# Optimization experiments

Measured on AMD Instinct MI355X. Metric: run time of the kernel, lower is better.

The kernel has to match this reference:

```python
import jax, jax.numpy as jnp
import numpy as np

BETA = 0.95
THR = 1.0  # snntorch Leaky default threshold

# Heaviside spike with ATan surrogate gradient (snntorch default, alpha=2):
# d/dx = 1 / (1 + (pi*x)^2)
@jax.custom_vjp
def spike_fn(x):
    return (x > 0).astype(x.dtype)

def _spike_fwd(x):
    return spike_fn(x), x

def _spike_bwd(x, g):
    return (g / (1.0 + (jnp.pi * x) ** 2),)

spike_fn.defvjp(_spike_fwd, _spike_bwd)


def setup_inputs() -> dict:
    key = jax.random.key(0)
    ks = jax.random.split(key, 5)
    T, B, D_in, D_h, D_out = 25, 4096, 784, 1000, 10
    x = jax.random.normal(ks[0], (T, B, D_in), dtype=jnp.float32)
    # Kaiming-uniform-ish init like nn.Linear
    w1 = jax.random.uniform(ks[1], (D_h, D_in), jnp.float32, -1, 1) / np.sqrt(D_in)
    b1 = jax.random.uniform(ks[2], (D_h,), jnp.float32, -1, 1) / np.sqrt(D_in)
    w2 = jax.random.uniform(ks[3], (D_out, D_h), jnp.float32, -1, 1) / np.sqrt(D_h)
    b2 = jax.random.uniform(ks[4], (D_out,), jnp.float32, -1, 1) / np.sqrt(D_h)
    return {"x": x, "w1": w1, "b1": b1, "w2": w2, "b2": b2}


def reference(x, w1, b1, w2, b2):
    B = x.shape[1]
    mem1_0 = jnp.zeros((B, w1.shape[0]), x.dtype)
    mem2_0 = jnp.zeros((B, w2.shape[0]), x.dtype)

    def step(carry, xt):
        mem1, mem2 = carry
        # layer 1: Linear + Leaky (reset-by-subtraction, reset from prior mem)
        cur1 = xt @ w1.T + b1
        reset1 = spike_fn(mem1 - THR)
        mem1 = BETA * mem1 + cur1 - reset1 * THR
        spk1 = spike_fn(mem1 - THR)
        # layer 2
        cur2 = spk1 @ w2.T + b2
        reset2 = spike_fn(mem2 - THR)
        mem2 = BETA * mem2 + cur2 - reset2 * THR
        spk2 = spike_fn(mem2 - THR)
        return (mem1, mem2), spk2

    (mem1, mem2), spk_rec = jax.lax.scan(step, (mem1_0, mem2_0), x)
    return spk_rec, mem2
```

## Files before the change

### kernel.cpp

```cpp
#include <hip/hip_runtime.h>

typedef _Float16 f16;
typedef _Float16 f16x4 __attribute__((ext_vector_type(4)));
typedef _Float16 f16x8 __attribute__((ext_vector_type(8)));
typedef float f32x4 __attribute__((ext_vector_type(4)));

#define T_STEPS 25
#define BATCH   4096
#define DIN     784
#define DH      1000
#define HP      1024
#define DOUT    10
#define MROWS   (T_STEPS * BATCH)
#define KSEG    800
#define KA      (2 * KSEG)
#define KB      (3 * KSEG)
#define WROW    2432
#define NT64    38

__global__ void aconv_kernel(const float* __restrict__ x, f16* __restrict__ Ah)
{
    const int total = MROWS * 200;
    for (int idx = blockIdx.x * blockDim.x + threadIdx.x; idx < total;
         idx += gridDim.x * blockDim.x) {
        const int r  = idx / 200;
        const int c4 = (idx - r * 200) * 4;
        f16x4 hi, lo;
        if (c4 < DIN) {
            const float4 v = *(const float4*)(x + (size_t)r * DIN + c4);
            const float vv[4] = {v.x, v.y, v.z, v.w};
            #pragma unroll
            for (int j = 0; j < 4; ++j) {
                f16 h = (f16)vv[j];
                hi[j] = h;
                lo[j] = (f16)(vv[j] - (float)h);
            }
        } else {
            #pragma unroll
            for (int j = 0; j < 4; ++j) { hi[j] = (f16)0.f; lo[j] = (f16)0.f; }
        }
        *(f16x4*)(Ah + (size_t)r * KA + c4)        = hi;
        *(f16x4*)(Ah + (size_t)r * KA + KSEG + c4) = lo;
    }
}

__global__ void wconv_kernel(const float* __restrict__ w1, const float* __restrict__ b1,
                             const float* __restrict__ w2,
                             f16* __restrict__ Wh, float* __restrict__ b1p,
                             float* __restrict__ w2t)
{
    const int stride = gridDim.x * blockDim.x;
    const int tid0 = blockIdx.x * blockDim.x + threadIdx.x;
    for (int idx = tid0; idx < HP * WROW; idx += stride) {
        const int n  = idx / WROW;
        const int k  = idx - n * WROW;
        f16 v = (f16)0.f;
        if (k < KB) {
            const int seg = k / KSEG;
            const int kc  = k - seg * KSEG;
            float w = (n < DH && kc < DIN) ? w1[n * DIN + kc] : 0.f;
            f16 h = (f16)w;
            v = (seg < 2) ? h : (f16)(w - (float)h);
        }
        Wh[idx] = v;
    }
    for (int idx = tid0; idx < HP; idx += stride)
        b1p[idx] = (idx < DH) ? b1[idx] : 0.f;
    for (int idx = tid0; idx < HP * DOUT; idx += stride) {
        const int h = idx / DOUT;
        const int o = idx - h * DOUT;
        w2t[idx] = (h < DH) ? w2[o * DH + h] : 0.f;
    }
}

#define GL(gp, ldsoff) __builtin_amdgcn_global_load_lds( \
    (const __attribute__((address_space(1))) void*)(gp), \
    (__attribute__((address_space(3))) void*)(lds + (ldsoff)), 16, 0, 0)

#define STAGE64(tt) do { \
    const int _buf = ((tt) & 1) * 16384; \
    const int _ak  = (((tt) < 25) ? (tt) : ((tt) - 25)) * 64; \
    const int _bk  = (tt) * 64; \
    GL(Ag + _ak + 0 * 64 * KA,   _buf + 0 * 4096 + widoff); \
    GL(Ag + _ak + 1 * 64 * KA,   _buf + 1 * 4096 + widoff); \
    GL(Ag + _ak + 2 * 64 * KA,   _buf + 2 * 4096 + widoff); \
    GL(Ag + _ak + 3 * 64 * KA,   _buf + 3 * 4096 + widoff); \
    GL(Bg + _bk + 0 * 64 * WROW, 32768 + _buf + 0 * 4096 + widoff); \
    GL(Bg + _bk + 1 * 64 * WROW, 32768 + _buf + 1 * 4096 + widoff); \
    GL(Bg + _bk + 2 * 64 * WROW, 32768 + _buf + 2 * 4096 + widoff); \
    GL(Bg + _bk + 3 * 64 * WROW, 32768 + _buf + 3 * 4096 + widoff); } while (0)

#define MFMA16(A0, A1, A2, A3, B0, B1, B2, B3, M0) \
    acc[M0+0][0] = __builtin_amdgcn_mfma_f32_16x16x32_f16(A0, B0, acc[M0+0][0], 0, 0, 0); \
    acc[M0+0][1] = __builtin_amdgcn_mfma_f32_16x16x32_f16(A0, B1, acc[M0+0][1], 0, 0, 0); \
    acc[M0+0][2] = __builtin_amdgcn_mfma_f32_16x16x32_f16(A0, B2, acc[M0+0][2], 0, 0, 0); \
    acc[M0+0][3] = __builtin_amdgcn_mfma_f32_16x16x32_f16(A0, B3, acc[M0+0][3], 0, 0, 0); \
    acc[M0+1][0] = __builtin_amdgcn_mfma_f32_16x16x32_f16(A1, B0, acc[M0+1][0], 0, 0, 0); \
    acc[M0+1][1] = __builtin_amdgcn_mfma_f32_16x16x32_f16(A1, B1, acc[M0+1][1], 0, 0, 0); \
    acc[M0+1][2] = __builtin_amdgcn_mfma_f32_16x16x32_f16(A1, B2, acc[M0+1][2], 0, 0, 0); \
    acc[M0+1][3] = __builtin_amdgcn_mfma_f32_16x16x32_f16(A1, B3, acc[M0+1][3], 0, 0, 0); \
    acc[M0+2][0] = __builtin_amdgcn_mfma_f32_16x16x32_f16(A2, B0, acc[M0+2][0], 0, 0, 0); \
    acc[M0+2][1] = __builtin_amdgcn_mfma_f32_16x16x32_f16(A2, B1, acc[M0+2][1], 0, 0, 0); \
    acc[M0+2][2] = __builtin_amdgcn_mfma_f32_16x16x32_f16(A2, B2, acc[M0+2][2], 0, 0, 0); \
    acc[M0+2][3] = __builtin_amdgcn_mfma_f32_16x16x32_f16(A2, B3, acc[M0+2][3], 0, 0, 0); \
    acc[M0+3][0] = __builtin_amdgcn_mfma_f32_16x16x32_f16(A3, B0, acc[M0+3][0], 0, 0, 0); \
    acc[M0+3][1] = __builtin_amdgcn_mfma_f32_16x16x32_f16(A3, B1, acc[M0+3][1], 0, 0, 0); \
    acc[M0+3][2] = __builtin_amdgcn_mfma_f32_16x16x32_f16(A3, B2, acc[M0+3][2], 0, 0, 0); \
    acc[M0+3][3] = __builtin_amdgcn_mfma_f32_16x16x32_f16(A3, B3, acc[M0+3][3], 0, 0, 0);

#define RD(off) (*(const f16x8*)(lds + (off)))

#define BODY64(tt, STG) do { \
    const int bufc = ((tt) & 1) * 16384; \
    f16x8 b00, b01, b02, b03, a00, a01, a02, a03, a10, a11, a12, a13; \
    f16x8 b10, b11, b12, b13, c00, c01, c02, c03, c10, c11, c12, c13; \
    if (STG) STAGE64((tt) + 1); \
     \
    b00 = RD(bbase + bufc + 0 * 1024 + cA0); \
    b01 = RD(bbase + bufc + 1 * 1024 + cA0); \
    b02 = RD(bbase + bufc + 2 * 1024 + cA0); \
    b03 = RD(bbase + bufc + 3 * 1024 + cA0); \
    a00 = RD(abase + bufc + 0 * 1024 + cA0); \
    a01 = RD(abase + bufc + 1 * 1024 + cA0); \
    a02 = RD(abase + bufc + 2 * 1024 + cA0); \
    a03 = RD(abase + bufc + 3 * 1024 + cA0); \
    a10 = RD(abase + bufc + 4096 + 0 * 1024 + cA0); \
    a11 = RD(abase + bufc + 4096 + 1 * 1024 + cA0); \
    a12 = RD(abase + bufc + 4096 + 2 * 1024 + cA0); \
    a13 = RD(abase + bufc + 4096 + 3 * 1024 + cA0); \
    asm volatile("s_waitcnt lgkmcnt(4)" ::: "memory");   \
    __builtin_amdgcn_sched_barrier(0); \
    __builtin_amdgcn_s_setprio(1); \
    MFMA16(a00, a01, a02, a03, b00, b01, b02, b03, 0) \
    __builtin_amdgcn_s_setprio(0); \
    asm volatile("s_waitcnt lgkmcnt(0)" ::: "memory");   \
    __builtin_amdgcn_sched_barrier(0); \
     \
    b10 = RD(bbase + bufc + 0 * 1024 + cA1); \
    b11 = RD(bbase + bufc + 1 * 1024 + cA1); \
    b12 = RD(bbase + bufc + 2 * 1024 + cA1); \
    b13 = RD(bbase + bufc + 3 * 1024 + cA1); \
    c00 = RD(abase + bufc + 0 * 1024 + cA1); \
    c01 = RD(abase + bufc + 1 * 1024 + cA1); \
    c02 = RD(abase + bufc + 2 * 1024 + cA1); \
    c03 = RD(abase + bufc + 3 * 1024 + cA1); \
    c10 = RD(abase + bufc + 4096 + 0 * 1024 + cA1); \
    c11 = RD(abase + bufc + 4096 + 1 * 1024 + cA1); \
    c12 = RD(abase + bufc + 4096 + 2 * 1024 + cA1); \
    c13 = RD(abase + bufc + 4096 + 3 * 1024 + cA1); \
    __builtin_amdgcn_sched_barrier(0); \
    __builtin_amdgcn_s_setprio(1); \
    MFMA16(a10, a11, a12, a13, b00, b01, b02, b03, 4) \
    __builtin_amdgcn_s_setprio(0); \
    asm volatile("s_waitcnt lgkmcnt(4)" ::: "memory");   \
    __builtin_amdgcn_sched_barrier(0); \
    __builtin_amdgcn_s_setprio(1); \
    MFMA16(c00, c01, c02, c03, b10, b11, b12, b13, 0) \
    __builtin_amdgcn_s_setprio(0); \
    asm volatile("s_waitcnt lgkmcnt(0)" ::: "memory");   \
    __builtin_amdgcn_sched_barrier(0); \
    __builtin_amdgcn_s_setprio(1); \
    MFMA16(c10, c11, c12, c13, b10, b11, b12, b13, 4) \
    __builtin_amdgcn_s_setprio(0); \
    if (STG) { \
        asm volatile("s_waitcnt vmcnt(0)" ::: "memory");   \
        __builtin_amdgcn_s_barrier(); \
    } \
} while (0)

__global__ __launch_bounds__(512, 2)
void gemm_kernel(const f16* __restrict__ A, const f16* __restrict__ B,
                 const float* __restrict__ bias, float* __restrict__ C)
{
    __shared__ f16 lds[65536];

    const int bid = blockIdx.x;
    const int swz = (bid & 7) * 200 + (bid >> 3);
    const int mt = swz >> 2;
    const int nt = swz & 3;
    const size_t rowBase = (size_t)mt * 256;
    const int colBase = nt * 256;

    const int tid  = threadIdx.x;
    const int wid  = tid >> 6;
    const int lane = tid & 63;
    const int wm = wid >> 2;
    const int wn = wid & 3;

    const int gsw = (tid & 7) ^ ((tid >> 3) & 7);
    const f16* Ag = A + (rowBase + (tid >> 3)) * KA + gsw * 8;
    const f16* Bg = B + (size_t)(colBase + (tid >> 3)) * WROW + gsw * 8;
    const int widoff = wid * 512;

    const int cA0 = (((lane >> 4))     ^ (lane & 7)) * 8;
    const int cA1 = (((lane >> 4) + 4) ^ (lane & 7)) * 8;
    const int abase = (wm * 128 + (lane & 15)) * 64;
    const int bbase = 32768 + (wn * 64 + (lane & 15)) * 64;

    f32x4 acc[8][4];
    #pragma unroll
    for (int m = 0; m < 8; ++m)
        #pragma unroll
        for (int n = 0; n < 4; ++n)
            acc[m][n] = (f32x4){0.f, 0.f, 0.f, 0.f};

    STAGE64(0);
    asm volatile("s_waitcnt vmcnt(0)" ::: "memory");
    __builtin_amdgcn_s_barrier();

    for (int t = 0; t < 36; t += 2) {
        BODY64(t, 1);
        BODY64(t + 1, 1);
    }
    BODY64(36, 1);
    BODY64(37, 0);

    const int c_col0 = colBase + wn * 64 + (lane & 15);
    const size_t c_row0 = rowBase + wm * 128 + (lane >> 4) * 4;
    #pragma unroll
    for (int n = 0; n < 4; ++n) {
        const int gcol = c_col0 + n * 16;
        const float bv = bias[gcol];
        #pragma unroll
        for (int m = 0; m < 8; ++m) {
            const size_t grow = c_row0 + m * 16;
            #pragma unroll
            for (int r = 0; r < 4; ++r)
                C[(grow + r) * HP + gcol] = acc[m][n][r] + bv;
        }
    }
}

__global__ __launch_bounds__(256)
void phase2_kernel(const float* __restrict__ cur1, const float* __restrict__ w2t,
                   const float* __restrict__ b2, float* __restrict__ out)
{
    __shared__ float w2s[HP * DOUT];
    const int tid = threadIdx.x;
    for (int i = tid; i < HP * DOUT; i += 256) w2s[i] = w2t[i];

    const int lane = tid & 63;
    const int wave = tid >> 6;
    const int b = blockIdx.x * 4 + wave;

    float m1[16];
    #pragma unroll
    for (int i = 0; i < 16; ++i) m1[i] = 0.f;
    float m2[DOUT], b2r[DOUT];
    #pragma unroll
    for (int o = 0; o < DOUT; ++o) { m2[o] = 0.f; b2r[o] = b2[o]; }
    __syncthreads();

    for (int t = 0; t < T_STEPS; ++t) {
        const float* cr = cur1 + ((size_t)t * BATCH + b) * HP;
        float p[DOUT];
        #pragma unroll
        for (int o = 0; o < DOUT; ++o) p[o] = 0.f;

        #pragma unroll
        for (int c = 0; c < 4; ++c) {
            const float4 cu = *(const float4*)(cr + c * 256 + lane * 4);
            const float cv[4] = {cu.x, cu.y, cu.z, cu.w};
            #pragma unroll
            for (int j = 0; j < 4; ++j) {
                const float mo = m1[c * 4 + j];
                const float rs = (mo > 1.0f) ? 1.0f : 0.0f;
                const float mn = 0.95f * mo + cv[j] - rs;
                m1[c * 4 + j] = mn;
                if (mn > 1.0f) {
                    const float* wr = w2s + (c * 256 + lane * 4 + j) * DOUT;
                    #pragma unroll
                    for (int o = 0; o < DOUT; ++o) p[o] += wr[o];
                }
            }
        }
        #pragma unroll
        for (int o = 0; o < DOUT; ++o) {
            float v = p[o];
            #pragma unroll
            for (int msk = 32; msk > 0; msk >>= 1) v += __shfl_xor(v, msk, 64);
            p[o] = v;
        }
        #pragma unroll
        for (int o = 0; o < DOUT; ++o) {
            const float cur2 = p[o] + b2r[o];
            const float mo = m2[o];
            const float rs = (mo > 1.0f) ? 1.0f : 0.0f;
            m2[o] = 0.95f * mo + cur2 - rs;
        }
        if (lane < DOUT)
            out[(size_t)t * (BATCH * DOUT) + (size_t)b * DOUT + lane] =
                (m2[lane] > 1.0f) ? 1.0f : 0.0f;
    }
    if (lane < DOUT)
        out[(size_t)T_STEPS * BATCH * DOUT + (size_t)b * DOUT + lane] = m2[lane];
}

extern "C" void kernel_launch(void* const* d_in, const int* in_sizes, int n_in,
                              void* d_out, int out_size, void* d_ws, size_t ws_size,
                              hipStream_t stream)
{
    const float* x  = (const float*)d_in[0];
    const float* w1 = (const float*)d_in[1];
    const float* b1 = (const float*)d_in[2];
    const float* w2 = (const float*)d_in[3];
    const float* b2 = (const float*)d_in[4];
    float* out = (float*)d_out;

    char* wsb = (char*)d_ws;
    f16*   Ah   = (f16*)(wsb);
    f16*   Wh   = (f16*)(wsb + 327680000);
    float* cur1 = (float*)(wsb + 327680000 + 4980736);
    float* b1p  = (float*)(wsb + 327680000 + 4980736 + 419430400);
    float* w2t  = (float*)(wsb + 327680000 + 4980736 + 419430400 + 4096);

    aconv_kernel<<<4096, 256, 0, stream>>>(x, Ah);
    wconv_kernel<<<1024, 256, 0, stream>>>(w1, b1, w2, Wh, b1p, w2t);
    gemm_kernel<<<1600, 512, 0, stream>>>(Ah, Wh, b1p, cur1);
    phase2_kernel<<<1024, 256, 0, stream>>>(cur1, w2t, b2, out);
}
```

Before: 746.7 us.

## Fuse fp32-to-split-fp16 conversion of x into the GEMM A-tile staging

```diff
diff --git a/kernel.cpp b/kernel.cpp
--- a/kernel.cpp
+++ b/kernel.cpp
@@ -1,7 +1,6 @@
 #include <hip/hip_runtime.h>
 
 typedef _Float16 f16;
-typedef _Float16 f16x4 __attribute__((ext_vector_type(4)));
 typedef _Float16 f16x8 __attribute__((ext_vector_type(8)));
 typedef float f32x4 __attribute__((ext_vector_type(4)));
 
@@ -13,36 +12,9 @@
 #define DOUT    10
 #define MROWS   (T_STEPS * BATCH)
 #define KSEG    800
-#define KA      (2 * KSEG)
 #define KB      (3 * KSEG)
 #define WROW    2432
 #define NT64    38
-
-__global__ void aconv_kernel(const float* __restrict__ x, f16* __restrict__ Ah)
-{
-    const int total = MROWS * 200;
-    for (int idx = blockIdx.x * blockDim.x + threadIdx.x; idx < total;
-         idx += gridDim.x * blockDim.x) {
-        const int r  = idx / 200;
-        const int c4 = (idx - r * 200) * 4;
-        f16x4 hi, lo;
-        if (c4 < DIN) {
-            const float4 v = *(const float4*)(x + (size_t)r * DIN + c4);
-            const float vv[4] = {v.x, v.y, v.z, v.w};
-            #pragma unroll
-            for (int j = 0; j < 4; ++j) {
-                f16 h = (f16)vv[j];
-                hi[j] = h;
-                lo[j] = (f16)(vv[j] - (float)h);
-            }
-        } else {
-            #pragma unroll
-            for (int j = 0; j < 4; ++j) { hi[j] = (f16)0.f; lo[j] = (f16)0.f; }
-        }
-        *(f16x4*)(Ah + (size_t)r * KA + c4)        = hi;
-        *(f16x4*)(Ah + (size_t)r * KA + KSEG + c4) = lo;
-    }
-}
 
 __global__ void wconv_kernel(const float* __restrict__ w1, const float* __restrict__ b1,
                              const float* __restrict__ w2,
@@ -77,19 +49,81 @@
     (const __attribute__((address_space(1))) void*)(gp), \
     (__attribute__((address_space(3))) void*)(lds + (ldsoff)), 16, 0, 0)
 
-#define STAGE64(tt) do { \
+#define AKOF(tt) ((((tt) < 25) ? (tt) : ((tt) - 25)) * 64)
+
+#define STAGE_B(tt) do { \
     const int _buf = ((tt) & 1) * 16384; \
-    const int _ak  = (((tt) < 25) ? (tt) : ((tt) - 25)) * 64; \
     const int _bk  = (tt) * 64; \
-    GL(Ag + _ak + 0 * 64 * KA,   _buf + 0 * 4096 + widoff); \
-    GL(Ag + _ak + 1 * 64 * KA,   _buf + 1 * 4096 + widoff); \
-    GL(Ag + _ak + 2 * 64 * KA,   _buf + 2 * 4096 + widoff); \
-    GL(Ag + _ak + 3 * 64 * KA,   _buf + 3 * 4096 + widoff); \
     GL(Bg + _bk + 0 * 64 * WROW, 32768 + _buf + 0 * 4096 + widoff); \
     GL(Bg + _bk + 1 * 64 * WROW, 32768 + _buf + 1 * 4096 + widoff); \
     GL(Bg + _bk + 2 * 64 * WROW, 32768 + _buf + 2 * 4096 + widoff); \
     GL(Bg + _bk + 3 * 64 * WROW, 32768 + _buf + 3 * 4096 + widoff); } while (0)
 
+#define ACOL(tt, c_, ldc_) \
+    const int c_    = AKOF(tt) + gsw8; \
+    const int _sc   = (c_ < 800) ? c_ : (c_ - 800); \
+    const int ldc_  = (_sc < 784) ? _sc : 0;
+
+#define LOADA01(tt) do { ACOL(tt, _c, _ldc) \
+    fa00 = *(const f32x4*)(Xrow + 0 * 64 * DIN + _ldc); \
+    fa01 = *(const f32x4*)(Xrow + 0 * 64 * DIN + _ldc + 4); \
+    fa10 = *(const f32x4*)(Xrow + 1 * 64 * DIN + _ldc); \
+    fa11 = *(const f32x4*)(Xrow + 1 * 64 * DIN + _ldc + 4); } while (0)
+#define LOADA23(tt) do { ACOL(tt, _c, _ldc) \
+    fa20 = *(const f32x4*)(Xrow + 2 * 64 * DIN + _ldc); \
+    fa21 = *(const f32x4*)(Xrow + 2 * 64 * DIN + _ldc + 4); \
+    fa30 = *(const f32x4*)(Xrow + 3 * 64 * DIN + _ldc); \
+    fa31 = *(const f32x4*)(Xrow + 3 * 64 * DIN + _ldc + 4); } while (0)
+
+#define CVT8(w_, va, vb) do { \
+    _Pragma("unroll") \
+    for (int _j = 0; _j < 4; ++_j) { \
+        float _v = va[_j]; \
+        f16 _h = (f16)_v; \
+        f16 _l = (f16)(_v - (float)_h); \
+        w_[_j] = _pad ? (f16)0.f : (_lo ? _l : _h); \
+    } \
+    _Pragma("unroll") \
+    for (int _j = 0; _j < 4; ++_j) { \
+        float _v = vb[_j]; \
+        f16 _h = (f16)_v; \
+        f16 _l = (f16)(_v - (float)_h); \
+        w_[4 + _j] = _pad ? (f16)0.f : (_lo ? _l : _h); \
+    } } while (0)
+
+#define CVTWR(tt) do { ACOL(tt, _c, _ldcu) (void)_ldcu; \
+    const int _sc2  = (_c < 800) ? _c : (_c - 800); \
+    const bool _lo  = (_c >= 800); \
+    const bool _pad = (_sc2 >= 784); \
+    const int _wb   = ((tt) & 1) * 16384 + tid * 8; \
+    f16x8 w0, w1_, w2_, w3_; \
+    CVT8(w0,  fa00, fa01); CVT8(w1_, fa10, fa11); \
+    CVT8(w2_, fa20, fa21); CVT8(w3_, fa30, fa31); \
+    *(f16x8*)(lds + _wb + 0 * 4096) = w0; \
+    *(f16x8*)(lds + _wb + 1 * 4096) = w1_; \
+    *(f16x8*)(lds + _wb + 2 * 4096) = w2_; \
+    *(f16x8*)(lds + _wb + 3 * 4096) = w3_; } while (0)
+
+#define MFMA16(A0, A1, A2, A3, B0, B1, B2, B3) \
+    acc[0][0] = __builtin_amdgcn_mfma_f32_16x16x32_f16(A0, B0, acc[0][0], 0, 0, 0); \
+    acc[0][1] = __builtin_amdgcn_mfma_f32_16x16x32_f16(A0, B1, acc[0][1], 0, 0, 0); \
+    acc[0][2] = __builtin_amdgcn_mfma_f32_16x16x32_f16(A0, B2, acc[0][2], 0, 0, 0); \
+    acc[0][3] = __builtin_amdgcn_mfma_f32_16x16x32_f16(A0, B3, acc[0][3], 0, 0, 0); \
+    acc[1][0] = __builtin_amdgcn_mfma_f32_16x16x32_f16(A1, B0, acc[1][0], 0, 0, 0); \
+    acc[1][1] = __builtin_amdgcn_mfma_f32_16x16x32_f16(A1, B1, acc[1][1], 0, 0, 0); \
+    acc[1][2] = __builtin_amdgcn_mfma_f32_16x16x32_f16(A1, B2, acc[1][2], 0, 0, 0); \
+    acc[1][3] = __builtin_amdgcn_mfma_f32_16x16x32_f16(A1, B3, acc[1][3], 0, 0, 0); \
+    acc[2][0] = __builtin_amdgcn_mfma_f32_16x16x32_f16(A2, B0, acc[2][0], 0, 0, 0); \
+    acc[2][1] = __builtin_amdgcn_mfma_f32_16x16x32_f16(A2, B1, acc[2][1], 0, 0, 0); \
+    acc[2][2] = __builtin_amdgcn_mfma_f32_16x16x32_f16(A2, B2, acc[2][2], 0, 0, 0); \
+    acc[2][3] = __builtin_amdgcn_mfma_f32_16x16x32_f16(A2, B3, acc[2][3], 0, 0, 0); \
+    acc[3][0] = __builtin_amdgcn_mfma_f32_16x16x32_f16(A3, B0, acc[3][0], 0, 0, 0); \
+    acc[3][1] = __builtin_amdgcn_mfma_f32_16x16x32_f16(A3, B1, acc[3][1], 0, 0, 0); \
+    acc[3][2] = __builtin_amdgcn_mfma_f32_16x16x32_f16(A3, B2, acc[3][2], 0, 0, 0); \
+    acc[3][3] = __builtin_amdgcn_mfma_f32_16x16x32_f16(A3, B3, acc[3][3], 0, 0, 0); \
+    acc[4][0] = __builtin_amdgcn_mfma_f32_16x16x32_f16(A0, B0, acc[4][0], 0, 0, 0);
+
+#undef MFMA16
 #define MFMA16(A0, A1, A2, A3, B0, B1, B2, B3, M0) \
     acc[M0+0][0] = __builtin_amdgcn_mfma_f32_16x16x32_f16(A0, B0, acc[M0+0][0], 0, 0, 0); \
     acc[M0+0][1] = __builtin_amdgcn_mfma_f32_16x16x32_f16(A0, B1, acc[M0+0][1], 0, 0, 0); \
@@ -109,13 +143,17 @@
     acc[M0+3][3] = __builtin_amdgcn_mfma_f32_16x16x32_f16(A3, B3, acc[M0+3][3], 0, 0, 0);
 
 #define RD(off) (*(const f16x8*)(lds + (off)))
+#define LGKM(n) asm volatile("s_waitcnt lgkmcnt(" #n ")" ::: "memory")
+#define SB      __builtin_amdgcn_sched_barrier(0)
+#define P1      __builtin_amdgcn_s_setprio(1)
+#define P0      __builtin_amdgcn_s_setprio(0)
 
 #define BODY64(tt, STG) do { \
     const int bufc = ((tt) & 1) * 16384; \
-    f16x8 b00, b01, b02, b03, a00, a01, a02, a03, a10, a11, a12, a13; \
-    f16x8 b10, b11, b12, b13, c00, c01, c02, c03, c10, c11, c12, c13; \
-    if (STG) STAGE64((tt) + 1); \
-     \
+    f16x8 a00, a01, a02, a03, b00, b01, b02, b03; \
+    f16x8 a10, a11, a12, a13, b10, b11, b12, b13; \
+    f16x8 c00, c01, c02, c03, c10, c11, c12, c13; \
+    if (STG) { LOADA01((tt) + 1); STAGE_B((tt) + 1); } \
     b00 = RD(bbase + bufc + 0 * 1024 + cA0); \
     b01 = RD(bbase + bufc + 1 * 1024 + cA0); \
     b02 = RD(bbase + bufc + 2 * 1024 + cA0); \
@@ -124,18 +162,13 @@
     a01 = RD(abase + bufc + 1 * 1024 + cA0); \
     a02 = RD(abase + bufc + 2 * 1024 + cA0); \
     a03 = RD(abase + bufc + 3 * 1024 + cA0); \
-    a10 = RD(abase + bufc + 4096 + 0 * 1024 + cA0); \
-    a11 = RD(abase + bufc + 4096 + 1 * 1024 + cA0); \
-    a12 = RD(abase + bufc + 4096 + 2 * 1024 + cA0); \
-    a13 = RD(abase + bufc + 4096 + 3 * 1024 + cA0); \
-    asm volatile("s_waitcnt lgkmcnt(4)" ::: "memory");   \
-    __builtin_amdgcn_sched_barrier(0); \
-    __builtin_amdgcn_s_setprio(1); \
-    MFMA16(a00, a01, a02, a03, b00, b01, b02, b03, 0) \
-    __builtin_amdgcn_s_setprio(0); \
-    asm volatile("s_waitcnt lgkmcnt(0)" ::: "memory");   \
-    __builtin_amdgcn_sched_barrier(0); \
-     \
+    a10 = RD(abase + bufc + 4 * 1024 + cA0); \
+    a11 = RD(abase + bufc + 5 * 1024 + cA0); \
+    a12 = RD(abase + bufc + 6 * 1024 + cA0); \
+    a13 = RD(abase + bufc + 7 * 1024 + cA0); \
+    LGKM(8); SB; \
+    P1; MFMA16(a00, a01, a02, a03, b00, b01, b02, b03, 0) P0; \
+    LGKM(0); SB; \
     b10 = RD(bbase + bufc + 0 * 1024 + cA1); \
     b11 = RD(bbase + bufc + 1 * 1024 + cA1); \
     b12 = RD(bbase + bufc + 2 * 1024 + cA1); \
@@ -144,32 +177,27 @@
     c01 = RD(abase + bufc + 1 * 1024 + cA1); \
     c02 = RD(abase + bufc + 2 * 1024 + cA1); \
     c03 = RD(abase + bufc + 3 * 1024 + cA1); \
-    c10 = RD(abase + bufc + 4096 + 0 * 1024 + cA1); \
-    c11 = RD(abase + bufc + 4096 + 1 * 1024 + cA1); \
-    c12 = RD(abase + bufc + 4096 + 2 * 1024 + cA1); \
-    c13 = RD(abase + bufc + 4096 + 3 * 1024 + cA1); \
-    __builtin_amdgcn_sched_barrier(0); \
-    __builtin_amdgcn_s_setprio(1); \
-    MFMA16(a10, a11, a12, a13, b00, b01, b02, b03, 4) \
-    __builtin_amdgcn_s_setprio(0); \
-    asm volatile("s_waitcnt lgkmcnt(4)" ::: "memory");   \
-    __builtin_amdgcn_sched_barrier(0); \
-    __builtin_amdgcn_s_setprio(1); \
-    MFMA16(c00, c01, c02, c03, b10, b11, b12, b13, 0) \
-    __builtin_amdgcn_s_setprio(0); \
-    asm volatile("s_waitcnt lgkmcnt(0)" ::: "memory");   \
-    __builtin_amdgcn_sched_barrier(0); \
-    __builtin_amdgcn_s_setprio(1); \
-    MFMA16(c10, c11, c12, c13, b10, b11, b12, b13, 4) \
-    __builtin_amdgcn_s_setprio(0); \
+    c10 = RD(abase + bufc + 4 * 1024 + cA1); \
+    c11 = RD(abase + bufc + 5 * 1024 + cA1); \
+    c12 = RD(abase + bufc + 6 * 1024 + cA1); \
+    c13 = RD(abase + bufc + 7 * 1024 + cA1); \
+    SB; \
+    P1; MFMA16(a10, a11, a12, a13, b00, b01, b02, b03, 4) P0; \
+    if (STG) LOADA23((tt) + 1); \
+    LGKM(4); SB; \
+    P1; MFMA16(c00, c01, c02, c03, b10, b11, b12, b13, 0) P0; \
+    LGKM(0); SB; \
+    P1; MFMA16(c10, c11, c12, c13, b10, b11, b12, b13, 4) P0; \
     if (STG) { \
-        asm volatile("s_waitcnt vmcnt(0)" ::: "memory");   \
+        CVTWR((tt) + 1);                                    \
+        asm volatile("s_waitcnt lgkmcnt(0)" ::: "memory");  \
+        asm volatile("s_waitcnt vmcnt(0)" ::: "memory");    \
         __builtin_amdgcn_s_barrier(); \
     } \
 } while (0)
 
 __global__ __launch_bounds__(512, 2)
-void gemm_kernel(const f16* __restrict__ A, const f16* __restrict__ B,
+void gemm_kernel(const float* __restrict__ X, const f16* __restrict__ B,
                  const float* __restrict__ bias, float* __restrict__ C)
 {
     __shared__ f16 lds[65536];
@@ -187,9 +215,10 @@
     const int wm = wid >> 2;
     const int wn = wid & 3;
 
-    const int gsw = (tid & 7) ^ ((tid >> 3) & 7);
-    const f16* Ag = A + (rowBase + (tid >> 3)) * KA + gsw * 8;
-    const f16* Bg = B + (size_t)(colBase + (tid >> 3)) * WROW + gsw * 8;
+    const int trow = tid >> 3;
+    const int gsw8 = ((tid & 7) ^ (trow & 7)) * 8;
+    const float* Xrow = X + (rowBase + trow) * (size_t)DIN;
+    const f16* Bg = B + (size_t)(colBase + trow) * WROW + gsw8;
     const int widoff = wid * 512;
 
     const int cA0 = (((lane >> 4))     ^ (lane & 7)) * 8;
@@ -204,16 +233,17 @@
         for (int n = 0; n < 4; ++n)
             acc[m][n] = (f32x4){0.f, 0.f, 0.f, 0.f};
 
-    STAGE64(0);
+    f32x4 fa00, fa01, fa10, fa11, fa20, fa21, fa30, fa31;
+
+    LOADA01(0); LOADA23(0); STAGE_B(0);
+    CVTWR(0);
+    asm volatile("s_waitcnt lgkmcnt(0)" ::: "memory");
     asm volatile("s_waitcnt vmcnt(0)" ::: "memory");
     __builtin_amdgcn_s_barrier();
 
-    for (int t = 0; t < 36; t += 2) {
+    for (int t = 0; t < NT64 - 1; ++t)
         BODY64(t, 1);
-        BODY64(t + 1, 1);
-    }
-    BODY64(36, 1);
-    BODY64(37, 0);
+    BODY64(NT64 - 1, 0);
 
     const int c_col0 = colBase + wn * 64 + (lane & 15);
     const size_t c_row0 = rowBase + wm * 128 + (lane >> 4) * 4;
@@ -308,14 +338,12 @@
     float* out = (float*)d_out;
 
     char* wsb = (char*)d_ws;
-    f16*   Ah   = (f16*)(wsb);
-    f16*   Wh   = (f16*)(wsb + 327680000);
-    float* cur1 = (float*)(wsb + 327680000 + 4980736);
-    float* b1p  = (float*)(wsb + 327680000 + 4980736 + 419430400);
-    float* w2t  = (float*)(wsb + 327680000 + 4980736 + 419430400 + 4096);
-
-    aconv_kernel<<<4096, 256, 0, stream>>>(x, Ah);
+    f16*   Wh   = (f16*)(wsb);
+    float* cur1 = (float*)(wsb + 4980736);
+    float* b1p  = (float*)(wsb + 4980736 + 419430400);
+    float* w2t  = (float*)(wsb + 4980736 + 419430400 + 4096);
+
     wconv_kernel<<<1024, 256, 0, stream>>>(w1, b1, w2, Wh, b1p, w2t);
-    gemm_kernel<<<1600, 512, 0, stream>>>(Ah, Wh, b1p, cur1);
+    gemm_kernel<<<1600, 512, 0, stream>>>(x, Wh, b1p, cur1);
     phase2_kernel<<<1024, 256, 0, stream>>>(cur1, w2t, b2, out);
 }
```

After: 1.245 ms. 1.67x slower.
